# Kernel tuning notes

Measured on AMD Instinct MI355X. Metric: run time of the kernel, lower is better.

The kernel has to match this reference:

```python
import jax, jax.numpy as jnp
import numpy as np

K = 1024        # num_embeddings
D = 256         # embedding_dim
B, T = 64, 512  # batch, time -> N = 32768 flattened vectors
S = 5           # num_samples
DECAY = 0.999
EPS = 1e-5
COMMIT = 0.25


def setup_inputs() -> dict:
    key = jax.random.key(0)
    k1, k2 = jax.random.split(key)
    x = jax.random.normal(k1, (B, T, D), dtype=jnp.float32)
    # nn.init.uniform_(weight, -1/512, 1/512)
    embedding = jax.random.uniform(k2, (K, D), dtype=jnp.float32, minval=-1.0 / 512, maxval=1.0 / 512)
    ema_count = jnp.zeros((K,), dtype=jnp.float32)
    ema_weight = embedding  # buffer initialized as a clone of the weight
    return {"x": x, "embedding": embedding, "ema_count": ema_count, "ema_weight": ema_weight}


def reference(x, embedding, ema_count, ema_weight):
    N = x.shape[0] * x.shape[1]
    xf = x.reshape(-1, D)                      # [N, D]
    xf_sg = jax.lax.stop_gradient(xf)
    w = jax.lax.stop_gradient(embedding)       # [K, D]

    distances = (jnp.sum(w * w, axis=1)[None, :]
                 + jnp.sum(xf_sg * xf_sg, axis=1, keepdims=True)
                 - 2.0 * (xf_sg @ w.T))

    # categorical sampling with logits = -distances, S samples per row -> [S, N]
    skey = jax.random.key(42)
    samples = jax.random.categorical(skey, -distances, axis=-1, shape=(S, N))

    # mean of S one-hots without materializing [S, N, K] one-hot tensor
    encodings = jnp.zeros((N, K), dtype=jnp.float32).at[jnp.arange(N)[None, :], samples].add(1.0 / S)

    # EMA codebook update (training path; all under no_grad in torch)
    new_count = DECAY * ema_count + (1.0 - DECAY) * jnp.sum(encodings, axis=0)
    n = jnp.sum(new_count)
    new_count = (new_count + EPS) / (n + K * EPS) * n
    dw = encodings.T @ xf_sg                   # [K, D]
    new_weight = DECAY * ema_weight + (1.0 - DECAY) * dw
    new_embedding = new_weight / new_count[:, None]

    # gather with the UPDATED codebook, mean over samples -> [N, D]
    quantized = jnp.mean(new_embedding[samples], axis=0).reshape(x.shape)
    quantized = jax.lax.stop_gradient(quantized)

    e_latent_loss = jnp.mean((x - quantized) ** 2)
    loss = COMMIT * e_latent_loss

    quantized_st = x + jax.lax.stop_gradient(quantized - x)  # straight-through

    avg_probs = jnp.mean(encodings, axis=0)
    perplexity = jnp.exp(-jnp.sum(avg_probs * jnp.log(avg_probs + 1e-10)))

    return quantized_st, loss, perplexity, new_embedding, new_count, new_weight
```

## Files before the change

### kernel.cpp

```cpp
#include <hip/hip_runtime.h>
#include <stdint.h>
#include <math.h>

#define NV 32768
#define DIM 256
#define KCB 1024
#define NSAMP 5

typedef double f64x4 __attribute__((ext_vector_type(4)));

__device__ __forceinline__ uint32_t rotl32(uint32_t v, int r) {
  return (v << r) | (v >> (32 - r));
}

__device__ __forceinline__ void threefry2x32(uint32_t c0, uint32_t c1,
                                             uint32_t& o0, uint32_t& o1) {
  const uint32_t k0 = 0u, k1 = 42u;
  const uint32_t k2 = k0 ^ k1 ^ 0x1BD11BDAu;
  uint32_t x0 = c0 + k0, x1 = c1 + k1;
  x0 += x1; x1 = rotl32(x1, 13); x1 ^= x0;
  x0 += x1; x1 = rotl32(x1, 15); x1 ^= x0;
  x0 += x1; x1 = rotl32(x1, 26); x1 ^= x0;
  x0 += x1; x1 = rotl32(x1,  6); x1 ^= x0;
  x0 += k1; x1 += k2 + 1u;
  x0 += x1; x1 = rotl32(x1, 17); x1 ^= x0;
  x0 += x1; x1 = rotl32(x1, 29); x1 ^= x0;
  x0 += x1; x1 = rotl32(x1, 16); x1 ^= x0;
  x0 += x1; x1 = rotl32(x1, 24); x1 ^= x0;
  x0 += k2; x1 += k0 + 2u;
  x0 += x1; x1 = rotl32(x1, 13); x1 ^= x0;
  x0 += x1; x1 = rotl32(x1, 15); x1 ^= x0;
  x0 += x1; x1 = rotl32(x1, 26); x1 ^= x0;
  x0 += x1; x1 = rotl32(x1,  6); x1 ^= x0;
  x0 += k0; x1 += k1 + 3u;
  x0 += x1; x1 = rotl32(x1, 17); x1 ^= x0;
  x0 += x1; x1 = rotl32(x1, 29); x1 ^= x0;
  x0 += x1; x1 = rotl32(x1, 16); x1 ^= x0;
  x0 += x1; x1 = rotl32(x1, 24); x1 ^= x0;
  x0 += k1; x1 += k2 + 4u;
  x0 += x1; x1 = rotl32(x1, 13); x1 ^= x0;
  x0 += x1; x1 = rotl32(x1, 15); x1 ^= x0;
  x0 += x1; x1 = rotl32(x1, 26); x1 ^= x0;
  x0 += x1; x1 = rotl32(x1,  6); x1 ^= x0;
  x0 += k2; x1 += k0 + 5u;
  o0 = x0; o1 = x1;
}

__device__ __forceinline__ float neg_log_f32(float xf) {
  uint32_t i = __float_as_uint(xf);
  int e = ((int)(i - 0x3f3504f3u)) >> 23;
  double m = (double)__uint_as_float(i - (uint32_t)(e << 23));
  double z = (m - 1.0) / (m + 1.0);
  double p = z * z;
  double poly = 0x1.1111111111111p-4;
  poly = fma(poly, p, 0x1.3b13b13b13b14p-4);
  poly = fma(poly, p, 0x1.745d1745d1746p-4);
  poly = fma(poly, p, 0x1.c71c71c71c71cp-4);
  poly = fma(poly, p, 0x1.2492492492492p-3);
  poly = fma(poly, p, 0x1.999999999999ap-3);
  poly = fma(poly, p, 0x1.5555555555555p-2);
  poly = fma(poly, p, 1.0);
  double r = fma(-2.0 * z, poly, (double)(-e) * 0x1.62e42fefa39efp-1);
  return (float)r;
}

__device__ __forceinline__ float u_from_bits(uint32_t bits) {
  uint32_t m = bits >> 9;
  return (m == 0u) ? 1.17549435e-38f
                   : (__uint_as_float(m | 0x3f800000u) - 1.0f);
}

__device__ __forceinline__ float gumbel_exact(uint32_t bits) {
  float u = u_from_bits(bits);
  float t = neg_log_f32(u);
  return neg_log_f32(t);
}

__device__ __forceinline__ float gumbel_approx(uint32_t bits) {
  float u = u_from_bits(bits);
  float t = __log2f(u) * (-0.6931471805599453f);
  return __log2f(t) * (-0.6931471805599453f);
}

#define E2G 4e-5f

__device__ __forceinline__ float thr_from(float wvt, float lvmax) {
  float y = wvt - lvmax - (E2G + 1e-4f);
  float t = __expf(-y);
  float thr = __expf(-t);
  return thr * 0.99998f;
}


__global__ __launch_bounds__(256) void k_prep32(const float* __restrict__ emb,
                                                float* __restrict__ wT) {
  __shared__ float tile[64][65];
  int bk = blockIdx.x;
  int bd = blockIdx.y;
  int t = threadIdx.x;
  int tr = t >> 6, tc = t & 63;
#pragma unroll
  for (int i = 0; i < 16; ++i) {
    int kk = tr + i * 4;
    tile[kk][tc] = emb[(size_t)(bk * 64 + kk) * 256 + bd * 64 + tc];
  }
  __syncthreads();
#pragma unroll
  for (int i = 0; i < 16; ++i) {
    int dd = tr + i * 4;
    wT[(size_t)(bd * 64 + dd) * 1024 + bk * 64 + tc] = tile[tc][dd];
  }
}

__global__ __launch_bounds__(256) void k_prep64(const float* __restrict__ emb,
                                                double* __restrict__ wT64) {
  __shared__ float tile[64][65];
  int bk = blockIdx.x;
  int bd = blockIdx.y;
  int t = threadIdx.x;
  int tr = t >> 6, tc = t & 63;
#pragma unroll
  for (int i = 0; i < 16; ++i) {
    int kk = tr + i * 4;
    tile[kk][tc] = emb[(size_t)(bk * 64 + kk) * 256 + bd * 64 + tc];
  }
  __syncthreads();
#pragma unroll
  for (int i = 0; i < 16; ++i) {
    int dd = tr + i * 4;
    wT64[(size_t)(bd * 64 + dd) * 1024 + bk * 64 + tc] = (double)tile[tc][dd];
  }
}

__global__ __launch_bounds__(256) void k_rowsumsq(const float* __restrict__ a,
                                                  float* __restrict__ outp,
                                                  int rows) {
  int r = blockIdx.x * blockDim.x + threadIdx.x;
  if (r >= rows) return;
  const float* p = a + (size_t)r * DIM;
  float acc = 0.0f;
  for (int i = 0; i < DIM; ++i) {
    float pi = p[i];
    acc = __fadd_rn(acc, __fmul_rn(pi, pi));
  }
  outp[r] = acc;
}


__global__ __launch_bounds__(256) void k_logits(const float* __restrict__ x,
                                                const float* __restrict__ wT,
                                                const float* __restrict__ wsum,
                                                float* __restrict__ logits,
                                                int chunkbase) {
  __shared__ float xl[32 * 260];
  __shared__ float xs[32];
  int nb = blockIdx.x;
  int t = threadIdx.x;
  int lane = t & 63, wv = t >> 6;
  int m = lane & 15, g = lane >> 4;
  int rg = wv >> 1, chf = wv & 1;

#pragma unroll
  for (int i = 0; i < 32; ++i)
    xl[i * 260 + t] = x[((size_t)(chunkbase + nb * 32) + i) * 256 + t];
  __syncthreads();

  if (t < 32) {
    const float* p = xl + t * 260;
    float acc = 0.0f;
    for (int i = 0; i < DIM; ++i) {
      float pi = p[i];
      acc = __fadd_rn(acc, __fmul_rn(pi, pi));
    }
    xs[t] = acc;
  }
  __syncthreads();

  const float* ap = xl + (rg * 16 + m) * 260 + g;
  for (int ch = 0; ch < 4; ++ch) {
    for (int ct = 0; ct < 8; ++ct) {
      int klocal = chf * 128 + ct * 16 + m;
      int kglob = ch * 256 + klocal;
      f64x4 C = {0.0, 0.0, 0.0, 0.0};
      const float* bp = wT + (size_t)g * 1024 + kglob;
#pragma unroll 8
      for (int step = 0; step < 64; ++step) {
        double a = (double)ap[step * 4];
        double b = (double)bp[(size_t)step * 4096];
        C = __builtin_amdgcn_mfma_f64_16x16x4f64(a, b, C, 0, 0, 0);
      }
      float ws_k = wsum[kglob];
#pragma unroll
      for (int j = 0; j < 4; ++j) {
        int rloc = rg * 16 + g * 4 + j;
        float l32 = __fsub_rn(__fmul_rn(2.0f, (float)C[j]),
                              __fadd_rn(ws_k, xs[rloc]));
        logits[(size_t)(nb * 32 + rloc) * 1024 + kglob] = l32;
      }
    }
  }
}

__global__ __launch_bounds__(256) void k_sampler(const float* __restrict__ logits,
                                                 int* __restrict__ samples,
                                                 int* __restrict__ cnt,
                                                 int chunkbase) {
  int t = threadIdx.x;
  int p = t & 15;
  int rloc = blockIdx.x * 16 + (t >> 4);
  int row = chunkbase + rloc;
  uint32_t rowk = (uint32_t)row * 1024u;

  const float4* lp = (const float4*)(logits + (size_t)rloc * 1024) + p;

  float lmax = -INFINITY;
#pragma unroll 1
  for (int j = 0; j < 16; ++j) {
    float4 f = lp[j * 16];
    lmax = fmaxf(lmax, fmaxf(fmaxf(f.x, f.y), fmaxf(f.z, f.w)));
  }
#pragma unroll
  for (int off = 1; off < 16; off <<= 1)
    lmax = fmaxf(lmax, __shfl_xor(lmax, off, 64));

  float    wvt[NSAMP], wlv[NSAMP], rlv[NSAMP], thr[NSAMP];
  int      wk[NSAMP], rk[NSAMP];
  uint32_t wbits[NSAMP], rbits[NSAMP];
  uint32_t rmask = 0;
#pragma unroll
  for (int s = 0; s < NSAMP; ++s) {
    wvt[s] = -INFINITY; wlv[s] = 0.f; wk[s] = 0; wbits[s] = 0u;
    rlv[s] = 0.f; rk[s] = 0; rbits[s] = 0u;
    thr[s] = -1.0f;
  }

#pragma unroll 1
  for (int j = 0; j < 16; ++j) {
    float4 f = lp[j * 16];
    float lvs[4] = {f.x, f.y, f.z, f.w};
    int kb = 4 * p + 64 * j;
#pragma unroll
    for (int e = 0; e < 4; ++e) {
      int k = kb + e;
      uint32_t cbase = rowk + (uint32_t)k;
#pragma unroll
      for (int s = 0; s < NSAMP; ++s) {
        uint32_t o0, o1;
        threefry2x32(0u, cbase + (uint32_t)s * 33554432u, o0, o1);
        uint32_t bits = o0 ^ o1;
        float uscr = __uint_as_float((bits >> 9) | 0x3f800000u) - 1.0f;
        if (uscr > thr[s]) {
          float lv = lvs[e];
          float vt = __fadd_rn(gumbel_approx(bits), lv);
          float wpre = wvt[s];
          if (fminf(vt, wpre) > fmaxf(vt, wpre) - E2G) {
            if (vt > wpre) { rk[s] = wk[s]; rbits[s] = wbits[s]; rlv[s] = wlv[s]; }
            else           { rk[s] = k;     rbits[s] = bits;     rlv[s] = lv; }
            rmask |= (1u << s);
          }
          bool gt = vt > wpre;
          wvt[s]   = gt ? vt   : wpre;
          wk[s]    = gt ? k    : wk[s];
          wbits[s] = gt ? bits : wbits[s];
          wlv[s]   = gt ? lv   : wlv[s];
          if (gt) thr[s] = thr_from(wvt[s], lmax);
        }
      }
    }
  }

#pragma unroll
  for (int s = 0; s < NSAMP; ++s) {
    float ev = __fadd_rn(gumbel_exact(wbits[s]), wlv[s]);
    int ek = wk[s];
    if (rmask & (1u << s)) {
      float er = __fadd_rn(gumbel_exact(rbits[s]), rlv[s]);
      if (er > ev || (er == ev && rk[s] < ek)) { ev = er; ek = rk[s]; }
    }
#pragma unroll
    for (int off = 1; off < 16; off <<= 1) {
      float v2 = __shfl_xor(ev, off, 64);
      int   k2 = __shfl_xor(ek, off, 64);
      if (v2 > ev || (v2 == ev && k2 < ek)) { ev = v2; ek = k2; }
    }
    if (p == 0) {
      samples[s * NV + row] = ek;
      atomicAdd(&cnt[ek], 1);
    }
  }
}

__global__ __launch_bounds__(256) void k_fused(const float* __restrict__ x,
                                               const double* __restrict__ wT64,
                                               const float* __restrict__ wsum,
                                               const float* __restrict__ xsum,
                                               int* __restrict__ samples,
                                               int* __restrict__ cnt) {
  __shared__ float xl[16 * 260];
  __shared__ float ll[256 * 17];
  __shared__ float xs[16];
  __shared__ float vred[4 * 16 * 5];
  __shared__ int   kred[4 * 16 * 5];

  int nb = blockIdx.x;
  int t = threadIdx.x;
  int lane = t & 63, wv = t >> 6;
  int m = lane & 15, g = lane >> 4;
  int r = t & 15, kg = t >> 4;

#pragma unroll
  for (int i = 0; i < 16; ++i)
    xl[i * 260 + t] = x[((size_t)nb * 16 + i) * 256 + t];
  if (t < 16) xs[t] = xsum[nb * 16 + t];
  __syncthreads();

  float    wvt[NSAMP], wlv[NSAMP], rlv[NSAMP];
  int      wk[NSAMP], rk[NSAMP];
  uint32_t wbits[NSAMP], rbits[NSAMP];
  uint32_t rvmask = 0;
#pragma unroll
  for (int s = 0; s < NSAMP; ++s) {
    wvt[s] = -INFINITY; wlv[s] = 0.f; wk[s] = 0; wbits[s] = 0u;
    rlv[s] = 0.f; rk[s] = 0; rbits[s] = 0u;
  }
  uint32_t rowbase = ((uint32_t)nb * 16u + (uint32_t)r) * 1024u;

  for (int ch = 0; ch < 4; ++ch) {
    for (int ct = 0; ct < 4; ++ct) {
      int klocal = wv * 64 + ct * 16 + m;
      int kglob = ch * 256 + klocal;
      f64x4 C = {0.0, 0.0, 0.0, 0.0};
      const double* bp = wT64 + (size_t)g * 1024 + kglob;
      const float* ap = xl + m * 260 + g;
#pragma unroll 8
      for (int step = 0; step < 64; ++step) {
        double a = (double)ap[step * 4];
        double b = bp[(size_t)step * 4096];
        C = __builtin_amdgcn_mfma_f64_16x16x4f64(a, b, C, 0, 0, 0);
      }
      float ws_k = wsum[kglob];
#pragma unroll
      for (int j = 0; j < 4; ++j) {
        int row = g * 4 + j;
        float l32 = __fsub_rn(__fmul_rn(2.0f, (float)C[j]),
                              __fadd_rn(ws_k, xs[row]));
        ll[klocal * 17 + row] = l32;
      }
    }
    __syncthreads();
#pragma unroll 1
    for (int i = 0; i < 16; ++i) {
      int kl = kg + (i << 4);
      float lv = ll[kl * 17 + r];
      int gki = (ch << 8) + kl;
      uint32_t cbase = rowbase + (uint32_t)gki;
#pragma unroll
      for (int s = 0; s < NSAMP; ++s) {
        uint32_t o0, o1;
        threefry2x32(0u, cbase + (uint32_t)s * 33554432u, o0, o1);
        uint32_t bits = o0 ^ o1;
        float vt = __fadd_rn(gumbel_approx(bits), lv);
        if (vt > wvt[s]) {
          if (wvt[s] > vt - E2G) {
            rk[s] = wk[s]; rbits[s] = wbits[s]; rlv[s] = wlv[s];
            rvmask |= (1u << s);
          }
          wvt[s] = vt; wk[s] = gki; wbits[s] = bits; wlv[s] = lv;
        } else if (vt > wvt[s] - E2G) {
          rk[s] = gki; rbits[s] = bits; rlv[s] = lv;
          rvmask |= (1u << s);
        }
      }
    }
    __syncthreads();
  }

#pragma unroll
  for (int s = 0; s < NSAMP; ++s) {
    float ev = __fadd_rn(gumbel_exact(wbits[s]), wlv[s]);
    int ek = wk[s];
    if (rvmask & (1u << s)) {
      float er = __fadd_rn(gumbel_exact(rbits[s]), rlv[s]);
      if (er > ev || (er == ev && rk[s] < ek)) { ev = er; ek = rk[s]; }
    }
#pragma unroll
    for (int off = 16; off <= 32; off <<= 1) {
      float v2 = __shfl_xor(ev, off, 64);
      int   k2 = __shfl_xor(ek, off, 64);
      if (v2 > ev || (v2 == ev && k2 < ek)) { ev = v2; ek = k2; }
    }
    if (g == 0) {
      vred[(wv * 16 + r) * 5 + s] = ev;
      kred[(wv * 16 + r) * 5 + s] = ek;
    }
  }
  __syncthreads();
  if (t < 80) {
    int rr = t / 5, s = t % 5;
    float best = vred[rr * 5 + s];
    int bk2 = kred[rr * 5 + s];
#pragma unroll
    for (int w = 1; w < 4; ++w) {
      float v2 = vred[(w * 16 + rr) * 5 + s];
      int   k2 = kred[(w * 16 + rr) * 5 + s];
      if (v2 > best || (v2 == best && k2 < bk2)) { best = v2; bk2 = k2; }
    }
    int n = nb * 16 + rr;
    samples[s * NV + n] = bk2;
    atomicAdd(&cnt[bk2], 1);
  }
}


__global__ __launch_bounds__(1024) void k_meta(const float* __restrict__ ema_count,
                                               const int* __restrict__ cnt,
                                               int* __restrict__ offs,
                                               int* __restrict__ cursor,
                                               double* __restrict__ ncn64,
                                               float* __restrict__ out_count,
                                               float* __restrict__ out_perp) {
  __shared__ int sc[1024];
  __shared__ double red[1024];
  int k = threadIdx.x;
  int v = cnt[k];
  sc[k] = v;
  __syncthreads();
  for (int off = 1; off < 1024; off <<= 1) {
    int a = (k >= off) ? sc[k - off] : 0;
    __syncthreads();
    sc[k] += a;
    __syncthreads();
  }
  int excl = sc[k] - v;
  offs[k] = excl;
  cursor[k] = excl;

  double ec = (double)v * 0.2;
  double nc0 = 0.999 * (double)ema_count[k] + 0.001 * ec;
  red[k] = nc0;
  __syncthreads();
  for (int off = 512; off > 0; off >>= 1) {
    if (k < off) red[k] += red[k + off];
    __syncthreads();
  }
  double ntot = red[0];
  __syncthreads();
  double ncn = (nc0 + 1e-5) / (ntot + (double)KCB * 1e-5) * ntot;
  ncn64[k] = ncn;
  out_count[k] = (float)ncn;

  double avg = ec / (double)NV;
  red[k] = avg * log(avg + 1e-10);
  __syncthreads();
  for (int off = 512; off > 0; off >>= 1) {
    if (k < off) red[k] += red[k + off];
    __syncthreads();
  }
  if (k == 0) out_perp[0] = (float)exp(-red[0]);
}

__global__ __launch_bounds__(256) void k_fill(const int* __restrict__ samples,
                                              int* __restrict__ cursor,
                                              uint32_t* __restrict__ list) {
  int idx = blockIdx.x * 256 + threadIdx.x;
  int k = samples[idx];
  int n = idx & (NV - 1);
  int pos = atomicAdd(&cursor[k], 1);
  list[pos] = (uint32_t)n;
}

__global__ __launch_bounds__(256) void k_weight2(const float* __restrict__ x,
                                                 const float* __restrict__ ema_w,
                                                 const uint32_t* __restrict__ list,
                                                 const int* __restrict__ offs,
                                                 const int* __restrict__ cnt,
                                                 const double* __restrict__ ncn64,
                                                 float* __restrict__ out_w,
                                                 float* __restrict__ out_emb,
                                                 float* __restrict__ emb32) {
  int k = blockIdx.x, d = threadIdx.x;
  const uint32_t* lp = list + offs[k];
  int mcnt = cnt[k];
  double acc0 = 0.0, acc1 = 0.0;
  int i = 0;
  for (; i + 2 <= mcnt; i += 2) {
    uint32_t n0 = lp[i], n1 = lp[i + 1];
    acc0 += (double)x[(size_t)n0 * 256 + d];
    acc1 += (double)x[(size_t)n1 * 256 + d];
  }
  if (i < mcnt) acc0 += (double)x[(size_t)lp[i] * 256 + d];
  double dw = 0.2 * (acc0 + acc1);
  double nw = 0.999 * (double)ema_w[(size_t)k * 256 + d] + 0.001 * dw;
  float nw32 = (float)nw;
  float e = __fdiv_rn(nw32, (float)ncn64[k]);
  size_t i2 = (size_t)k * 256 + d;
  out_w[i2] = nw32;
  out_emb[i2] = e;
  emb32[i2] = e;
}

__global__ __launch_bounds__(256) void k_quant(const float* __restrict__ x,
                                               const int* __restrict__ samples,
                                               const float* __restrict__ emb32,
                                               float* __restrict__ out_q,
                                               double* __restrict__ lossacc) {
  __shared__ int s5[16][5];
  __shared__ double wred[4];
  int bid = blockIdx.x;
  int t = threadIdx.x;
  if (t < 80) {
    int rr = t / 5, s = t % 5;
    s5[rr][s] = samples[s * NV + bid * 16 + rr];
  }
  __syncthreads();
  double lacc = 0.0;
#pragma unroll 1
  for (int rr = 0; rr < 16; ++rr) {
    size_t n = (size_t)bid * 16 + rr;
    float xv = x[n * DIM + t];
    float acc = emb32[(size_t)s5[rr][0] * DIM + t];
#pragma unroll
    for (int s = 1; s < NSAMP; ++s)
      acc = __fadd_rn(acc, emb32[(size_t)s5[rr][s] * DIM + t]);
    float q = __fdiv_rn(acc, 5.0f);
    out_q[n * DIM + t] = __fadd_rn(xv, __fsub_rn(q, xv));
    float df = __fsub_rn(xv, q);
    lacc += (double)df * (double)df;
  }
  for (int off = 32; off > 0; off >>= 1) lacc += __shfl_down(lacc, off, 64);
  int wid = t >> 6, lane = t & 63;
  if (lane == 0) wred[wid] = lacc;
  __syncthreads();
  if (t == 0) {
    double b = wred[0] + wred[1] + wred[2] + wred[3];
    __hip_atomic_fetch_add(lossacc, b, __ATOMIC_RELAXED, __HIP_MEMORY_SCOPE_AGENT);
  }
}

__global__ void k_loss(const double* __restrict__ lossacc,
                       float* __restrict__ out_loss) {
  out_loss[0] = (float)(0.25 * (lossacc[0] / (double)(NV * DIM)));
}

extern "C" void kernel_launch(void* const* d_in, const int* in_sizes, int n_in,
                              void* d_out, int out_size, void* d_ws, size_t ws_size,
                              hipStream_t stream) {
  const float* x     = (const float*)d_in[0];
  const float* emb   = (const float*)d_in[1];
  const float* ema_c = (const float*)d_in[2];
  const float* ema_w = (const float*)d_in[3];

  float* out      = (float*)d_out;
  float* out_q    = out;
  float* out_loss = out + 8388608;
  float* out_perp = out + 8388609;
  float* out_emb  = out + 8388610;
  float* out_cnt  = out + 8650754;
  float* out_w    = out + 8651778;

  char* ws = (char*)d_ws;

  float*    wT      = (float*)(ws + 0);
  float*    wsum    = (float*)(ws + 1048576);
  float*    xsum    = (float*)(ws + 1052672);
  int*      samples = (int*)(ws + 1183744);
  int*      cnt     = (int*)(ws + 1839104);
  double*   lossacc = (double*)(ws + 1843200);
  double*   ncn64   = (double*)(ws + 1843456);
  int*      offs    = (int*)(ws + 1851648);
  int*      cursor  = (int*)(ws + 1855744);
  uint32_t* list    = (uint32_t*)(ws + 1859840);
  float*    emb32   = (float*)(ws + 2515200);
  float*    logits  = (float*)(ws + 3563776);

  size_t avail = (ws_size > 3563776) ? (ws_size - 3563776) : 0;
  size_t maxr = (avail / 4096) & ~(size_t)31;
  int chunk_rows = (maxr > (size_t)NV) ? NV : (int)maxr;
  bool split = (chunk_rows >= 8192);

  if (split) {
    hipMemsetAsync(ws + 1839104, 0, 4096 + 8, stream);
    k_prep32<<<dim3(16, 4), 256, 0, stream>>>(emb, wT);
    k_rowsumsq<<<KCB / 256, 256, 0, stream>>>(emb, wsum, KCB);
    for (int base = 0; base < NV; base += chunk_rows) {
      int rows = (NV - base < chunk_rows) ? (NV - base) : chunk_rows;
      k_logits<<<rows / 32, 256, 0, stream>>>(x, wT, wsum, logits, base);
      k_sampler<<<rows / 16, 256, 0, stream>>>(logits, samples, cnt, base);
    }
    k_meta<<<1, 1024, 0, stream>>>(ema_c, cnt, offs, cursor, ncn64,
                                   out_cnt, out_perp);
    k_fill<<<NV * NSAMP / 256, 256, 0, stream>>>(samples, cursor, list);
    k_weight2<<<KCB, 256, 0, stream>>>(x, ema_w, list, offs, cnt, ncn64,
                                       out_w, out_emb, emb32);
    k_quant<<<NV / 16, 256, 0, stream>>>(x, samples, emb32, out_q, lossacc);
    k_loss<<<1, 1, 0, stream>>>(lossacc, out_loss);
  } else {
    double*   wT64_f    = (double*)(ws + 0);
    float*    wsum_f    = (float*)(ws + 2097152);
    float*    xsum_f    = (float*)(ws + 2101248);
    int*      samples_f = (int*)(ws + 2232320);
    int*      cnt_f     = (int*)(ws + 2887680);
    double*   lossacc_f = (double*)(ws + 2891776);
    double*   ncn64_f   = (double*)(ws + 2891784);
    int*      offs_f    = (int*)(ws + 2899976);
    int*      cursor_f  = (int*)(ws + 2904072);
    uint32_t* list_f    = (uint32_t*)(ws + 2908168);
    float*    emb32_f   = (float*)(ws + 3563528);

    hipMemsetAsync(ws + 2887680, 0, 4096 + 8, stream);
    k_prep64<<<dim3(16, 4), 256, 0, stream>>>(emb, wT64_f);
    k_rowsumsq<<<KCB / 256, 256, 0, stream>>>(emb, wsum_f, KCB);
    k_rowsumsq<<<NV / 256, 256, 0, stream>>>(x, xsum_f, NV);
    k_fused<<<NV / 16, 256, 0, stream>>>(x, wT64_f, wsum_f, xsum_f,
                                         samples_f, cnt_f);
    k_meta<<<1, 1024, 0, stream>>>(ema_c, cnt_f, offs_f, cursor_f, ncn64_f,
                                   out_cnt, out_perp);
    k_fill<<<NV * NSAMP / 256, 256, 0, stream>>>(samples_f, cursor_f, list_f);
    k_weight2<<<KCB, 256, 0, stream>>>(x, ema_w, list_f, offs_f, cnt_f, ncn64_f,
                                       out_w, out_emb, emb32_f);
    k_quant<<<NV / 16, 256, 0, stream>>>(x, samples_f, emb32_f, out_q, lossacc_f);
    k_loss<<<1, 1, 0, stream>>>(lossacc_f, out_loss);
  }
}
```

Before: 883.7 us.

## Replace fp64 MFMA distance GEMM with 3-way bf16-split MFMA emulation

The logits GEMM now splits x and the codebook into three bf16 parts each (hi/mid/lo) and accumulates six bf16 MFMA products in fp32, replacing the fp64 16x16x4 MFMA path. A new decomposition kernel produces the split operands and row norms. The sampler also drops the per-row max pass and threshold-based skipping, evaluating the approximate Gumbel for every candidate and reloading logits only for the final exact comparison. This trades fp64 matrix throughput for much faster bf16 MFMAs, at some risk of reduced accuracy near sampling ties and extra memory traffic for the split buffers.

```diff
diff --git a/kernel.cpp b/kernel.cpp
--- a/kernel.cpp
+++ b/kernel.cpp
@@ -8,6 +8,8 @@
 #define NSAMP 5
 
 typedef double f64x4 __attribute__((ext_vector_type(4)));
+typedef float  f32x4v __attribute__((ext_vector_type(4)));
+typedef short  bf16x8 __attribute__((ext_vector_type(8)));
 
 __device__ __forceinline__ uint32_t rotl32(uint32_t v, int r) {
   return (v << r) | (v >> (32 - r));
@@ -84,31 +86,44 @@
 
 #define E2G 4e-5f
 
-__device__ __forceinline__ float thr_from(float wvt, float lvmax) {
-  float y = wvt - lvmax - (E2G + 1e-4f);
-  float t = __expf(-y);
-  float thr = __expf(-t);
-  return thr * 0.99998f;
-}
-
-
-__global__ __launch_bounds__(256) void k_prep32(const float* __restrict__ emb,
-                                                float* __restrict__ wT) {
-  __shared__ float tile[64][65];
-  int bk = blockIdx.x;
-  int bd = blockIdx.y;
+__device__ __forceinline__ uint32_t f2bf(float f) {
+  uint32_t b = __float_as_uint(f);
+  return (b + 0x7fffu + ((b >> 16) & 1u)) >> 16;
+}
+__device__ __forceinline__ float bf2f(uint32_t h) {
+  return __uint_as_float(h << 16);
+}
+
+
+__global__ __launch_bounds__(256) void k_decomp(const float* __restrict__ src,
+                                                ushort* __restrict__ b0,
+                                                ushort* __restrict__ b1,
+                                                ushort* __restrict__ b2,
+                                                float* __restrict__ sums) {
+  __shared__ float xl[16 * 260];
+  int r0 = blockIdx.x * 16;
   int t = threadIdx.x;
-  int tr = t >> 6, tc = t & 63;
 #pragma unroll
   for (int i = 0; i < 16; ++i) {
-    int kk = tr + i * 4;
-    tile[kk][tc] = emb[(size_t)(bk * 64 + kk) * 256 + bd * 64 + tc];
-  }
-  __syncthreads();
-#pragma unroll
-  for (int i = 0; i < 16; ++i) {
-    int dd = tr + i * 4;
-    wT[(size_t)(bd * 64 + dd) * 1024 + bk * 64 + tc] = tile[tc][dd];
+    float v = src[(size_t)(r0 + i) * 256 + t];
+    xl[i * 260 + t] = v;
+    uint32_t h0 = f2bf(v);
+    float f0 = bf2f(h0);
+    float r1 = v - f0;
+    uint32_t h1 = f2bf(r1);
+    float f1 = bf2f(h1);
+    float r2 = r1 - f1;
+    uint32_t h2 = f2bf(r2);
+    size_t o = (size_t)(r0 + i) * 256 + t;
+    b0[o] = (ushort)h0; b1[o] = (ushort)h1; b2[o] = (ushort)h2;
+  }
+  __syncthreads();
+  if (t < 16) {
+    const float* p = xl + t * 260;
+    float acc = 0.0f;
+    for (int i = 0; i < 256; ++i)
+      acc = __fadd_rn(acc, __fmul_rn(p[i], p[i]));
+    sums[r0 + t] = acc;
   }
 }
 
@@ -147,55 +162,75 @@
 }
 
 
-__global__ __launch_bounds__(256) void k_logits(const float* __restrict__ x,
-                                                const float* __restrict__ wT,
-                                                const float* __restrict__ wsum,
-                                                float* __restrict__ logits,
-                                                int chunkbase) {
-  __shared__ float xl[32 * 260];
-  __shared__ float xs[32];
-  int nb = blockIdx.x;
+__global__ __launch_bounds__(256) void k_logits_bf(
+    const ushort* __restrict__ xb0, const ushort* __restrict__ xb1,
+    const ushort* __restrict__ xb2,
+    const ushort* __restrict__ wp0, const ushort* __restrict__ wp1,
+    const ushort* __restrict__ wp2,
+    const float* __restrict__ wsum, const float* __restrict__ xsum,
+    float* __restrict__ logits, int chunkbase) {
   int t = threadIdx.x;
-  int lane = t & 63, wv = t >> 6;
-  int m = lane & 15, g = lane >> 4;
-  int rg = wv >> 1, chf = wv & 1;
-
-#pragma unroll
-  for (int i = 0; i < 32; ++i)
-    xl[i * 260 + t] = x[((size_t)(chunkbase + nb * 32) + i) * 256 + t];
-  __syncthreads();
-
-  if (t < 32) {
-    const float* p = xl + t * 260;
-    float acc = 0.0f;
-    for (int i = 0; i < DIM; ++i) {
-      float pi = p[i];
-      acc = __fadd_rn(acc, __fmul_rn(pi, pi));
-    }
-    xs[t] = acc;
-  }
-  __syncthreads();
-
-  const float* ap = xl + (rg * 16 + m) * 260 + g;
-  for (int ch = 0; ch < 4; ++ch) {
-    for (int ct = 0; ct < 8; ++ct) {
-      int klocal = chf * 128 + ct * 16 + m;
-      int kglob = ch * 256 + klocal;
-      f64x4 C = {0.0, 0.0, 0.0, 0.0};
-      const float* bp = wT + (size_t)g * 1024 + kglob;
-#pragma unroll 8
-      for (int step = 0; step < 64; ++step) {
-        double a = (double)ap[step * 4];
-        double b = (double)bp[(size_t)step * 4096];
-        C = __builtin_amdgcn_mfma_f64_16x16x4f64(a, b, C, 0, 0, 0);
-      }
-      float ws_k = wsum[kglob];
-#pragma unroll
-      for (int j = 0; j < 4; ++j) {
-        int rloc = rg * 16 + g * 4 + j;
-        float l32 = __fsub_rn(__fmul_rn(2.0f, (float)C[j]),
-                              __fadd_rn(ws_k, xs[rloc]));
-        logits[(size_t)(nb * 32 + rloc) * 1024 + kglob] = l32;
+  int l = t & 63, wid = t >> 6;
+  int rows0 = blockIdx.x * 64 + wid * 16;
+  int lrow = l & 15, lk = l >> 4;
+
+  bf16x8 a0[8], a1[8], a2[8];
+  {
+    size_t rb = (size_t)(rows0 + lrow) * 256 + (size_t)lk * 8;
+#pragma unroll
+    for (int ch = 0; ch < 8; ++ch) {
+      a0[ch] = *reinterpret_cast<const bf16x8*>(xb0 + rb + ch * 32);
+      a1[ch] = *reinterpret_cast<const bf16x8*>(xb1 + rb + ch * 32);
+      a2[ch] = *reinterpret_cast<const bf16x8*>(xb2 + rb + ch * 32);
+    }
+  }
+  float xs4[4];
+#pragma unroll
+  for (int r = 0; r < 4; ++r)
+    xs4[r] = xsum[chunkbase + rows0 + lk * 4 + r];
+
+#pragma unroll 1
+  for (int strip = 0; strip < 16; ++strip) {
+    int col0 = strip * 64;
+    f32x4v acc0 = {0.f, 0.f, 0.f, 0.f};
+    f32x4v acc1 = {0.f, 0.f, 0.f, 0.f};
+    f32x4v acc2 = {0.f, 0.f, 0.f, 0.f};
+    f32x4v acc3 = {0.f, 0.f, 0.f, 0.f};
+
+#define KT_STEP(ACC, KT)                                                      \
+    {                                                                         \
+      size_t wb = (size_t)(col0 + (KT) * 16 + lrow) * 256 + ch * 32 + lk * 8; \
+      bf16x8 fb0 = *reinterpret_cast<const bf16x8*>(wp0 + wb);                \
+      bf16x8 fb1 = *reinterpret_cast<const bf16x8*>(wp1 + wb);                \
+      bf16x8 fb2 = *reinterpret_cast<const bf16x8*>(wp2 + wb);                \
+      ACC = __builtin_amdgcn_mfma_f32_16x16x32_bf16(a0[ch], fb0, ACC, 0,0,0); \
+      ACC = __builtin_amdgcn_mfma_f32_16x16x32_bf16(a0[ch], fb1, ACC, 0,0,0); \
+      ACC = __builtin_amdgcn_mfma_f32_16x16x32_bf16(a1[ch], fb0, ACC, 0,0,0); \
+      ACC = __builtin_amdgcn_mfma_f32_16x16x32_bf16(a1[ch], fb1, ACC, 0,0,0); \
+      ACC = __builtin_amdgcn_mfma_f32_16x16x32_bf16(a0[ch], fb2, ACC, 0,0,0); \
+      ACC = __builtin_amdgcn_mfma_f32_16x16x32_bf16(a2[ch], fb0, ACC, 0,0,0); \
+    }
+
+#pragma unroll
+    for (int ch = 0; ch < 8; ++ch) {
+      KT_STEP(acc0, 0)
+      KT_STEP(acc1, 1)
+      KT_STEP(acc2, 2)
+      KT_STEP(acc3, 3)
+    }
+#undef KT_STEP
+
+#pragma unroll
+    for (int kt = 0; kt < 4; ++kt) {
+      f32x4v acc = (kt == 0) ? acc0 : (kt == 1) ? acc1 : (kt == 2) ? acc2 : acc3;
+      int col = col0 + kt * 16 + lrow;
+      float ws_k = wsum[col];
+#pragma unroll
+      for (int r = 0; r < 4; ++r) {
+        int row = rows0 + lk * 4 + r;
+        float l32 = __fsub_rn(__fmul_rn(2.0f, acc[r]),
+                              __fadd_rn(ws_k, xs4[r]));
+        logits[(size_t)row * 1024 + col] = l32;
       }
     }
   }
@@ -213,68 +248,57 @@
 
   const float4* lp = (const float4*)(logits + (size_t)rloc * 1024) + p;
 
-  float lmax = -INFINITY;
-#pragma unroll 1
-  for (int j = 0; j < 16; ++j) {
-    float4 f = lp[j * 16];
-    lmax = fmaxf(lmax, fmaxf(fmaxf(f.x, f.y), fmaxf(f.z, f.w)));
-  }
-#pragma unroll
-  for (int off = 1; off < 16; off <<= 1)
-    lmax = fmaxf(lmax, __shfl_xor(lmax, off, 64));
-
-  float    wvt[NSAMP], wlv[NSAMP], rlv[NSAMP], thr[NSAMP];
+  float    wvt[NSAMP];
   int      wk[NSAMP], rk[NSAMP];
   uint32_t wbits[NSAMP], rbits[NSAMP];
   uint32_t rmask = 0;
 #pragma unroll
   for (int s = 0; s < NSAMP; ++s) {
-    wvt[s] = -INFINITY; wlv[s] = 0.f; wk[s] = 0; wbits[s] = 0u;
-    rlv[s] = 0.f; rk[s] = 0; rbits[s] = 0u;
-    thr[s] = -1.0f;
+    wvt[s] = -INFINITY; wk[s] = 0; wbits[s] = 0u; rk[s] = 0; rbits[s] = 0u;
   }
 
 #pragma unroll 1
   for (int j = 0; j < 16; ++j) {
-    float4 f = lp[j * 16];
+    float4 f = lp[(size_t)j * 16];
     float lvs[4] = {f.x, f.y, f.z, f.w};
     int kb = 4 * p + 64 * j;
 #pragma unroll
     for (int e = 0; e < 4; ++e) {
       int k = kb + e;
+      float lv = lvs[e];
       uint32_t cbase = rowk + (uint32_t)k;
 #pragma unroll
       for (int s = 0; s < NSAMP; ++s) {
         uint32_t o0, o1;
         threefry2x32(0u, cbase + (uint32_t)s * 33554432u, o0, o1);
         uint32_t bits = o0 ^ o1;
-        float uscr = __uint_as_float((bits >> 9) | 0x3f800000u) - 1.0f;
-        if (uscr > thr[s]) {
-          float lv = lvs[e];
-          float vt = __fadd_rn(gumbel_approx(bits), lv);
-          float wpre = wvt[s];
-          if (fminf(vt, wpre) > fmaxf(vt, wpre) - E2G) {
-            if (vt > wpre) { rk[s] = wk[s]; rbits[s] = wbits[s]; rlv[s] = wlv[s]; }
-            else           { rk[s] = k;     rbits[s] = bits;     rlv[s] = lv; }
-            rmask |= (1u << s);
-          }
-          bool gt = vt > wpre;
-          wvt[s]   = gt ? vt   : wpre;
-          wk[s]    = gt ? k    : wk[s];
-          wbits[s] = gt ? bits : wbits[s];
-          wlv[s]   = gt ? lv   : wlv[s];
-          if (gt) thr[s] = thr_from(wvt[s], lmax);
+        float u = __uint_as_float((bits >> 9) | 0x3f800000u) - 1.0f;
+        float tt = __log2f(u) * (-0.6931471805599453f);
+        float g  = __log2f(tt) * (-0.6931471805599453f);
+        float vt = __fadd_rn(g, lv);
+        float wpre = wvt[s];
+        float d = vt - wpre;
+        if (fabsf(d) < E2G) {
+          bool up = vt > wpre;
+          rk[s]    = up ? wk[s]    : k;
+          rbits[s] = up ? wbits[s] : bits;
+          rmask |= (1u << s);
         }
+        bool gt = vt > wpre;
+        wvt[s]   = gt ? vt   : wpre;
+        wk[s]    = gt ? k    : wk[s];
+        wbits[s] = gt ? bits : wbits[s];
       }
     }
   }
 
+  const float* lrow_p = logits + (size_t)rloc * 1024;
 #pragma unroll
   for (int s = 0; s < NSAMP; ++s) {
-    float ev = __fadd_rn(gumbel_exact(wbits[s]), wlv[s]);
+    float ev = __fadd_rn(gumbel_exact(wbits[s]), lrow_p[wk[s]]);
     int ek = wk[s];
     if (rmask & (1u << s)) {
-      float er = __fadd_rn(gumbel_exact(rbits[s]), rlv[s]);
+      float er = __fadd_rn(gumbel_exact(rbits[s]), lrow_p[rk[s]]);
       if (er > ev || (er == ev && rk[s] < ek)) { ev = er; ek = rk[s]; }
     }
 #pragma unroll
@@ -560,31 +584,41 @@
 
   char* ws = (char*)d_ws;
 
-  float*    wT      = (float*)(ws + 0);
-  float*    wsum    = (float*)(ws + 1048576);
-  float*    xsum    = (float*)(ws + 1052672);
-  int*      samples = (int*)(ws + 1183744);
-  int*      cnt     = (int*)(ws + 1839104);
-  double*   lossacc = (double*)(ws + 1843200);
-  double*   ncn64   = (double*)(ws + 1843456);
-  int*      offs    = (int*)(ws + 1851648);
-  int*      cursor  = (int*)(ws + 1855744);
-  uint32_t* list    = (uint32_t*)(ws + 1859840);
-  float*    emb32   = (float*)(ws + 2515200);
-  float*    logits  = (float*)(ws + 3563776);
-
-  size_t avail = (ws_size > 3563776) ? (ws_size - 3563776) : 0;
-  size_t maxr = (avail / 4096) & ~(size_t)31;
+  ushort*   wb0     = (ushort*)(ws + 0);
+  ushort*   wb1     = (ushort*)(ws + 524288);
+  ushort*   wb2     = (ushort*)(ws + 1048576);
+  float*    wsum    = (float*)(ws + 1572864);
+  float*    xsum    = (float*)(ws + 1576960);
+  int*      samples = (int*)(ws + 1708032);
+  int*      cnt     = (int*)(ws + 2363392);
+  double*   lossacc = (double*)(ws + 2367488);
+  double*   ncn64   = (double*)(ws + 2367496);
+  int*      offs    = (int*)(ws + 2375688);
+  int*      cursor  = (int*)(ws + 2379784);
+  uint32_t* list    = (uint32_t*)(ws + 2383880);
+  float*    emb32   = (float*)(ws + 3039240);
+  const size_t CB   = 4088064;
+
+  size_t avail = (ws_size > CB) ? (ws_size - CB) : 0;
+  size_t maxr = (avail / 5632) & ~(size_t)63;
   int chunk_rows = (maxr > (size_t)NV) ? NV : (int)maxr;
   bool split = (chunk_rows >= 8192);
 
   if (split) {
-    hipMemsetAsync(ws + 1839104, 0, 4096 + 8, stream);
-    k_prep32<<<dim3(16, 4), 256, 0, stream>>>(emb, wT);
-    k_rowsumsq<<<KCB / 256, 256, 0, stream>>>(emb, wsum, KCB);
+    ushort* xb0 = (ushort*)(ws + CB);
+    ushort* xb1 = xb0 + (size_t)chunk_rows * 256;
+    ushort* xb2 = xb1 + (size_t)chunk_rows * 256;
+    float*  logits = (float*)(ws + CB + (size_t)chunk_rows * 1536);
+
+    hipMemsetAsync(ws + 2363392, 0, 4104, stream);
+    k_decomp<<<KCB / 16, 256, 0, stream>>>(emb, wb0, wb1, wb2, wsum);
     for (int base = 0; base < NV; base += chunk_rows) {
       int rows = (NV - base < chunk_rows) ? (NV - base) : chunk_rows;
-      k_logits<<<rows / 32, 256, 0, stream>>>(x, wT, wsum, logits, base);
+      k_decomp<<<rows / 16, 256, 0, stream>>>(x + (size_t)base * 256,
+                                              xb0, xb1, xb2, xsum + base);
+      k_logits_bf<<<rows / 64, 256, 0, stream>>>(xb0, xb1, xb2,
+                                                 wb0, wb1, wb2,
+                                                 wsum, xsum, logits, base);
       k_sampler<<<rows / 16, 256, 0, stream>>>(logits, samples, cnt, base);
     }
     k_meta<<<1, 1024, 0, stream>>>(ema_c, cnt, offs, cursor, ncn64,
```

Result: no change. 874.1 us (-1.1%).
